# Optimization experiments

Measured on AMD Instinct MI355X. Metric: run time of the kernel, lower is better.

The kernel has to match this reference:

```python
import jax, jax.numpy as jnp
from jax import lax
import numpy as np

VOCAB, EMB = 50000, 300
HID, NCLS = 100, 20
BATCH, SEQ = 128, 512
P_DROP = 0.5


def setup_inputs() -> dict:
    key = jax.random.key(0)
    ks = jax.random.split(key, 8)
    s_e = 1.0 / np.sqrt(EMB)
    s_h = 1.0 / np.sqrt(HID)
    return {
        "inputs_batch": jax.random.randint(ks[0], (BATCH, SEQ), 0, VOCAB, dtype=jnp.int64)
        if jax.config.jax_enable_x64 else jax.random.randint(ks[0], (BATCH, SEQ), 0, VOCAB, dtype=jnp.int32),
        "emb_table": jax.random.normal(ks[1], (VOCAB, EMB), dtype=jnp.float32),
        # GRUCell params (torch layout): gates order [r, z, n]
        "w_ih": jax.random.uniform(ks[2], (3 * HID, EMB), jnp.float32, -s_h, s_h),
        "w_hh": jax.random.uniform(ks[3], (3 * HID, HID), jnp.float32, -s_h, s_h),
        "b_ih": jax.random.uniform(ks[4], (3 * HID,), jnp.float32, -s_h, s_h),
        "b_hh": jax.random.uniform(ks[5], (3 * HID,), jnp.float32, -s_h, s_h),
        "w_lin": jax.random.uniform(ks[6], (NCLS, HID), jnp.float32, -s_h, s_h),
        "b_lin": jax.random.uniform(ks[7], (NCLS,), jnp.float32, -s_h, s_h),
    }


def reference(inputs_batch, emb_table, w_ih, w_hh, b_ih, b_hh, w_lin, b_lin):
    B, S = inputs_batch.shape
    H = w_hh.shape[1]
    keep = 1.0 - P_DROP
    dk1, dk2 = jax.random.split(jax.random.key(42))

    z_embed = emb_table[inputs_batch]                       # [B, S, E]
    m1 = jax.random.bernoulli(dk1, keep, z_embed.shape)     # dropout1 mask
    z_embed = jnp.where(m1, z_embed / keep, 0.0)
    x_seq = jnp.swapaxes(z_embed, 0, 1)                     # [S, B, E]
    m2 = jax.random.bernoulli(dk2, keep, (S, B, H))         # per-step dropout2 masks

    def step(h, inp):
        x, m = inp
        gi = x @ w_ih.T + b_ih                              # [B, 3H]
        gh = h @ w_hh.T + b_hh
        i_r, i_z, i_n = jnp.split(gi, 3, axis=-1)
        h_r, h_z, h_n = jnp.split(gh, 3, axis=-1)
        r = jax.nn.sigmoid(i_r + h_r)
        zg = jax.nn.sigmoid(i_z + h_z)
        n = jnp.tanh(i_n + r * h_n)
        h_new = (1.0 - zg) * n + zg * h
        h_d = jnp.where(m, h_new / keep, 0.0)
        y = jax.nn.log_softmax(h_d @ w_lin.T + b_lin, axis=1)  # [B, C]
        return h_new, y

    h0 = jnp.zeros((B, H), dtype=x_seq.dtype)
    _, ys = lax.scan(step, h0, (x_seq, m2))                 # ys: [S, B, C]
    return jnp.transpose(ys, (1, 2, 0))                     # [B, C, S]
```

## Files before the change

kernel.cpp:

```cpp
#include <hip/hip_runtime.h>
#include <hip/hip_bf16.h>
#include <cstdint>

#define BATCH 128
#define SEQ   512
#define EMB   300
#define HID   100
#define G3    300
#define NCLS  20
#define NROWS (SEQ * BATCH)

#define M1_WORDS 614400
#define M2_WORDS 204800

typedef __attribute__((ext_vector_type(4))) float f32x4;
typedef __attribute__((ext_vector_type(8))) short s16x8;
typedef __fp16 h16x2 __attribute__((ext_vector_type(2)));

__host__ __device__ __forceinline__ void threefry2x32(uint32_t k0, uint32_t k1,
                                                      uint32_t x0, uint32_t x1,
                                                      uint32_t* o0, uint32_t* o1) {
  uint32_t ks2 = k0 ^ k1 ^ 0x1BD11BDAu;
  x0 += k0; x1 += k1;
#define TFR(r) { x0 += x1; x1 = (x1 << (r)) | (x1 >> (32 - (r))); x1 ^= x0; }
  TFR(13) TFR(15) TFR(26) TFR(6)  x0 += k1;  x1 += ks2 + 1u;
  TFR(17) TFR(29) TFR(16) TFR(24) x0 += ks2; x1 += k0 + 2u;
  TFR(13) TFR(15) TFR(26) TFR(6)  x0 += k0;  x1 += k1 + 3u;
  TFR(17) TFR(29) TFR(16) TFR(24) x0 += k1;  x1 += ks2 + 4u;
  TFR(13) TFR(15) TFR(26) TFR(6)  x0 += ks2; x1 += k0 + 5u;
#undef TFR
  *o0 = x0; *o1 = x1;
}

__device__ __forceinline__ uint32_t rand_bits32(uint32_t ka, uint32_t kb, uint32_t flat) {
  uint32_t a, b;
  threefry2x32(ka, kb, 0u, flat, &a, &b);
  return a ^ b;
}

__device__ __forceinline__ short f2bf(float f) {
  union { float f; uint32_t u; } c; c.f = f;
  uint32_t u = c.u;
  return (short)((u + 0x7FFFu + ((u >> 16) & 1u)) >> 16);
}

__device__ __forceinline__ void bar_lds() {
  __asm__ __volatile__("s_waitcnt lgkmcnt(0)" ::: "memory");
  __builtin_amdgcn_s_barrier();
  __asm__ __volatile__("" ::: "memory");
}

__global__ __launch_bounds__(256) void k_mask(uint32_t* __restrict__ M1w,
                                              uint32_t* __restrict__ M2w,
                                              uint32_t k1a, uint32_t k1b,
                                              uint32_t k2a, uint32_t k2b) {
  const int i = blockIdx.x * 256 + threadIdx.x;
  uint32_t ka, kb, base;
  uint32_t* dst;
  if (i < M1_WORDS) { ka = k1a; kb = k1b; base = (uint32_t)i * 32u; dst = M1w + i; }
  else { ka = k2a; kb = k2b; base = (uint32_t)(i - M1_WORDS) * 32u; dst = M2w + (i - M1_WORDS); }
  uint32_t w = 0u;
#pragma unroll
  for (int j = 0; j < 32; ++j) {
    uint32_t bits = rand_bits32(ka, kb, base + (uint32_t)j);
    w |= ((~bits) >> 31) << j;
  }
  *dst = w;
}

__global__ __launch_bounds__(256) void k_prepw(const float* __restrict__ w_ih,
                                               short* __restrict__ Wb) {
  int i8 = (blockIdx.x * 256 + threadIdx.x) * 8;
  if (i8 >= 304 * 320) return;
  short o[8];
#pragma unroll
  for (int j = 0; j < 8; ++j) {
    int pos = i8 + j;
    int n = pos / 320, k = pos - (pos / 320) * 320;
    float v = (n < 300 && k < 300) ? w_ih[(size_t)n * EMB + k] : 0.f;
    o[j] = f2bf(v);
  }
  *(s16x8*)(Wb + i8) = *(s16x8*)o;
}

__global__ __launch_bounds__(512) void k_gi7(const int* __restrict__ inputs,
                                             const float* __restrict__ emb,
                                             const short* __restrict__ Wb,
                                             const float* __restrict__ b_ih,
                                             const uint32_t* __restrict__ M1w,
                                             float* __restrict__ GI) {
  __shared__ short As[128 * 40];
  __shared__ short Bs[304 * 40];
  __shared__ int idxs[128];
  const int t = threadIdx.x;
  const int s = blockIdx.x;
  const int lane = t & 63, wave = t >> 6;
  const int wr = wave & 1;
  const int wc = wave >> 1;
  const int ml = lane & 15, quad = lane >> 4;
  const int arow = t >> 2;
  const int akq = t & 3;

  if (t < 128) idxs[t] = inputs[t * SEQ + s];
  __syncthreads();

  const int nfr = (wc < 3) ? 5 : 4;
  f32x4 acc[4][5];
#pragma unroll
  for (int i = 0; i < 4; ++i)
#pragma unroll
    for (int j = 0; j < 5; ++j) acc[i][j] = (f32x4){0.f, 0.f, 0.f, 0.f};

  const int myidx = idxs[arow];

  for (int c = 0; c < 10; ++c) {
    const int e0 = c * 32 + akq * 8;
    float xa[8];
#pragma unroll
    for (int j = 0; j < 8; ++j) xa[j] = 0.f;
    if (e0 + 7 < 300) {
#pragma unroll
      for (int q4 = 0; q4 < 2; ++q4) {
        float4 v = *(const float4*)(emb + (size_t)myidx * EMB + e0 + q4 * 4);
        xa[q4 * 4 + 0] = v.x; xa[q4 * 4 + 1] = v.y; xa[q4 * 4 + 2] = v.z; xa[q4 * 4 + 3] = v.w;
      }
    } else if (e0 < 300) {
#pragma unroll
      for (int j = 0; j < 8; ++j) {
        int e = e0 + j;
        if (e < 300) xa[j] = emb[(size_t)myidx * EMB + e];
      }
    }
    uint32_t mb = 0;
    if (e0 < 300) {
      uint32_t base = (uint32_t)((arow * SEQ + s) * EMB + e0);
      uint64_t mw = (uint64_t)M1w[base >> 5] | ((uint64_t)M1w[(base >> 5) + 1] << 32);
      mb = (uint32_t)(mw >> (base & 31));
    }
    short sa[8];
#pragma unroll
    for (int j = 0; j < 8; ++j)
      sa[j] = f2bf(((mb >> j) & 1u) ? xa[j] * 2.f : 0.f);
    s16x8 bv0, bv1, bv2;
    {
      int i0 = t;
      bv0 = *(const s16x8*)(Wb + (size_t)(i0 >> 2) * 320 + c * 32 + (i0 & 3) * 8);
      int i1 = t + 512;
      bv1 = *(const s16x8*)(Wb + (size_t)(i1 >> 2) * 320 + c * 32 + (i1 & 3) * 8);
      if (t < 192) {
        int i2 = t + 1024;
        bv2 = *(const s16x8*)(Wb + (size_t)(i2 >> 2) * 320 + c * 32 + (i2 & 3) * 8);
      }
    }
    if (c > 0) __syncthreads();
    *(s16x8*)&As[arow * 40 + akq * 8] = *(s16x8*)&sa[0];
    {
      int i0 = t;       *(s16x8*)&Bs[(i0 >> 2) * 40 + (i0 & 3) * 8] = bv0;
      int i1 = t + 512; *(s16x8*)&Bs[(i1 >> 2) * 40 + (i1 & 3) * 8] = bv1;
      if (t < 192) { int i2 = t + 1024; *(s16x8*)&Bs[(i2 >> 2) * 40 + (i2 & 3) * 8] = bv2; }
    }
    __syncthreads();
    s16x8 af[4];
#pragma unroll
    for (int mt = 0; mt < 4; ++mt)
      af[mt] = *(const s16x8*)&As[(wr * 64 + mt * 16 + ml) * 40 + quad * 8];
#pragma unroll
    for (int j = 0; j < 5; ++j) {
      if (j < nfr) {
        int nt = wc + 4 * j;
        s16x8 bf = *(const s16x8*)&Bs[(nt * 16 + ml) * 40 + quad * 8];
#pragma unroll
        for (int mt = 0; mt < 4; ++mt)
          acc[mt][j] = __builtin_amdgcn_mfma_f32_16x16x32_bf16(af[mt], bf, acc[mt][j], 0, 0, 0);
      }
    }
  }

#pragma unroll
  for (int j = 0; j < 5; ++j) {
    if (j < nfr) {
      int n = (wc + 4 * j) * 16 + ml;
      if (n < 300) {
        float bias = b_ih[n];
#pragma unroll
        for (int mt = 0; mt < 4; ++mt) {
#pragma unroll
          for (int i = 0; i < 4; ++i) {
            int brow = wr * 64 + mt * 16 + quad * 4 + i;
            GI[(size_t)(s * BATCH + brow) * G3 + n] = acc[mt][j][i] + bias;
          }
        }
      }
    }
  }
}

__global__ __launch_bounds__(512, 1) void k_rnn12(const float* __restrict__ GI,
                                                  const float* __restrict__ w_hh,
                                                  const float* __restrict__ b_hh,
                                                  const uint8_t* __restrict__ M2,
                                                  float* __restrict__ Hd) {
  __shared__ __align__(16) uint32_t hp_s[2][64];
  const int t = threadIdx.x, b = blockIdx.x;
  const int u = t >> 2, ks = t & 3;
  const bool act = (u < 100);
  const bool gate = act && (ks == 0);
  const int uc = act ? u : 99;
  const int kplo = (ks < 2) ? ks * 13 : 26 + (ks - 2) * 12;
  const int np = (ks < 2) ? 13 : 12;

  const float* rowR = w_hh + (size_t)uc * HID;
  const float* rowZ = w_hh + (size_t)(uc + 100) * HID;
  const float* rowN = w_hh + (size_t)(uc + 200) * HID;
  const h16x2 z2 = (h16x2){(__fp16)0.f, (__fp16)0.f};
  h16x2 wR[13], wZ[13], wN[13];
#pragma unroll
  for (int j = 0; j < 13; ++j) {
    if (j < np) {
      int o = 2 * (kplo + j);
      wR[j] = __builtin_amdgcn_cvt_pkrtz(rowR[o], rowR[o + 1]);
      wZ[j] = __builtin_amdgcn_cvt_pkrtz(rowZ[o], rowZ[o + 1]);
      wN[j] = __builtin_amdgcn_cvt_pkrtz(rowN[o], rowN[o + 1]);
    } else { wR[j] = z2; wZ[j] = z2; wN[j] = z2; }
  }

  float bR0 = 0.f, bZ0 = 0.f, bN0 = 0.f;
  float gcR = 0.f, gcZ = 0.f, gcN = 0.f;
  float g1R = 0.f, g1Z = 0.f, g1N = 0.f;
  uint8_t mc = 0, m1 = 0;
  if (gate) {
    bR0 = b_hh[u]; bZ0 = b_hh[100 + u]; bN0 = b_hh[200 + u];
    const float* g0 = GI + (size_t)b * G3;
    gcR = g0[u]; gcZ = g0[100 + u]; gcN = g0[200 + u];
    mc = M2[(uint32_t)(b * HID + u) >> 3];
    const float* gp1 = GI + (size_t)(BATCH + b) * G3;
    g1R = gp1[u]; g1Z = gp1[100 + u]; g1N = gp1[200 + u];
    m1 = M2[(uint32_t)((BATCH + b) * HID + u) >> 3];
  }
  const int p = u >> 1;
  const int sidx = (p < 13) ? 0 : (p < 26) ? 1 : (p < 38) ? 2 : 3;
  const int spos = p - ((sidx < 2) ? sidx * 13 : 26 + (sidx - 2) * 12);
  const int hidx = (sidx * 16 + spos) * 2 + (u & 1);

  if (t < 128) ((uint32_t*)hp_s)[t] = 0u;
  float hprev = 0.f;
  __syncthreads();

#define QPX(x, c) __builtin_bit_cast(float, __builtin_amdgcn_mov_dpp( \
    __builtin_bit_cast(int, (x)), (c), 0xF, 0xF, true))
#define DOT_S(J, W) { h16x2 hh = __builtin_bit_cast(h16x2, (W)); \
    sR = __builtin_amdgcn_fdot2(wR[J], hh, sR, false); \
    sZ = __builtin_amdgcn_fdot2(wZ[J], hh, sZ, false); \
    sN = __builtin_amdgcn_fdot2(wN[J], hh, sN, false); }
#define DOT_T(J, W) { h16x2 hh = __builtin_bit_cast(h16x2, (W)); \
    tR = __builtin_amdgcn_fdot2(wR[J], hh, tR, false); \
    tZ = __builtin_amdgcn_fdot2(wZ[J], hh, tZ, false); \
    tN = __builtin_amdgcn_fdot2(wN[J], hh, tN, false); }

#pragma unroll 2
  for (int s = 0; s < SEQ; ++s) {
    float g2R = 0.f, g2Z = 0.f, g2N = 0.f;
    uint8_t m2b = 0;
    if (gate) {
      int sn = (s + 2 < SEQ) ? s + 2 : SEQ - 1;
      const float* gp = GI + (size_t)(sn * BATCH + b) * G3;
      g2R = gp[u]; g2Z = gp[100 + u]; g2N = gp[200 + u];
      m2b = M2[(uint32_t)((sn * BATCH + b) * HID + u) >> 3];
    }
    if (act) {
      float sR = bR0, sZ = bZ0, sN = bN0;
      float tR = 0.f, tZ = 0.f, tN = 0.f;
      const uint32_t* hb = &hp_s[s & 1][0] + (ks << 4);
      uint4 h0 = *(const uint4*)hb;
      uint4 h1 = *(const uint4*)(hb + 4);
      uint4 h2 = *(const uint4*)(hb + 8);
      uint32_t h3 = hb[12];
      DOT_S(0, h0.x)  DOT_S(1, h0.y)  DOT_S(2, h0.z)  DOT_S(3, h0.w)
      DOT_S(4, h1.x)  DOT_S(5, h1.y)
      DOT_T(6, h1.z)  DOT_T(7, h1.w)
      DOT_T(8, h2.x)  DOT_T(9, h2.y)  DOT_T(10, h2.z) DOT_T(11, h2.w)
      DOT_T(12, h3)
      sR += tR; sZ += tZ; sN += tN;
      sR += QPX(sR, 0xB1); sZ += QPX(sZ, 0xB1); sN += QPX(sN, 0xB1);
      sR += QPX(sR, 0x4E); sZ += QPX(sZ, 0x4E); sN += QPX(sN, 0x4E);
      if (gate) {
        float r = 1.f / (1.f + __expf(-(gcR + sR)));
        float z = 1.f / (1.f + __expf(-(gcZ + sZ)));
        float xn = gcN + r * sN;
        float e2 = __expf(2.f * fabsf(xn));
        float n = copysignf(1.f - 2.f / (e2 + 1.f), xn);
        float hnew = (1.f - z) * n + z * hprev;
        hprev = hnew;
        uint32_t fl = (uint32_t)((s * BATCH + b) * HID + u);
        float hd = ((mc >> (fl & 7)) & 1u) ? hnew * 2.f : 0.f;
        Hd[(size_t)(b * SEQ + s) * HID + u] = hd;
        ((__fp16*)&hp_s[(s & 1) ^ 1][0])[hidx] = (__fp16)hnew;
      }
    }
    gcR = g1R; gcZ = g1Z; gcN = g1N; mc = m1;
    g1R = g2R; g1Z = g2Z; g1N = g2N; m1 = m2b;
    bar_lds();
  }
#undef DOT_S
#undef DOT_T
#undef QPX
}

__global__ __launch_bounds__(64) void k_out(const float* __restrict__ Hd,
                                            const float* __restrict__ w_lin,
                                            const float* __restrict__ b_lin,
                                            float* __restrict__ out) {
  __shared__ float Wl[NCLS * HID];
  __shared__ float bl[NCLS];
  const int t = threadIdx.x;
  for (int i = t; i < NCLS * HID; i += 64) Wl[i] = w_lin[i];
  if (t < NCLS) bl[t] = b_lin[t];
  __syncthreads();

  const int r0 = (blockIdx.x * 64 + t) * 4;
  float acc[4][NCLS];
#pragma unroll
  for (int r = 0; r < 4; ++r)
#pragma unroll
    for (int c = 0; c < NCLS; ++c) acc[r][c] = bl[c];

  for (int k = 0; k < HID; k += 4) {
    float4 h0 = *(const float4*)(Hd + (size_t)(r0 + 0) * HID + k);
    float4 h1 = *(const float4*)(Hd + (size_t)(r0 + 1) * HID + k);
    float4 h2 = *(const float4*)(Hd + (size_t)(r0 + 2) * HID + k);
    float4 h3 = *(const float4*)(Hd + (size_t)(r0 + 3) * HID + k);
#pragma unroll
    for (int c = 0; c < NCLS; ++c) {
      float4 w4 = *(const float4*)&Wl[c * HID + k];
      acc[0][c] += h0.x * w4.x + h0.y * w4.y + h0.z * w4.z + h0.w * w4.w;
      acc[1][c] += h1.x * w4.x + h1.y * w4.y + h1.z * w4.z + h1.w * w4.w;
      acc[2][c] += h2.x * w4.x + h2.y * w4.y + h2.z * w4.z + h2.w * w4.w;
      acc[3][c] += h3.x * w4.x + h3.y * w4.y + h3.z * w4.z + h3.w * w4.w;
    }
  }

  float lse[4];
#pragma unroll
  for (int r = 0; r < 4; ++r) {
    float mx = acc[r][0];
#pragma unroll
    for (int c = 1; c < NCLS; ++c) mx = fmaxf(mx, acc[r][c]);
    float se = 0.f;
#pragma unroll
    for (int c = 0; c < NCLS; ++c) se += __expf(acc[r][c] - mx);
    lse[r] = mx + __logf(se);
  }
  const int b = r0 >> 9, s0 = r0 & 511;
#pragma unroll
  for (int c = 0; c < NCLS; ++c) {
    float4 o = make_float4(acc[0][c] - lse[0], acc[1][c] - lse[1],
                           acc[2][c] - lse[2], acc[3][c] - lse[3]);
    *(float4*)(out + (size_t)(b * NCLS + c) * SEQ + s0) = o;
  }
}

extern "C" void kernel_launch(void* const* d_in, const int* in_sizes, int n_in,
                              void* d_out, int out_size, void* d_ws, size_t ws_size,
                              hipStream_t stream) {
  const int*   inputs = (const int*)d_in[0];
  const float* emb    = (const float*)d_in[1];
  const float* w_ih   = (const float*)d_in[2];
  const float* w_hh   = (const float*)d_in[3];
  const float* b_ih   = (const float*)d_in[4];
  const float* b_hh   = (const float*)d_in[5];
  const float* w_lin  = (const float*)d_in[6];
  const float* b_lin  = (const float*)d_in[7];
  float* out = (float*)d_out;

  float* GI = (float*)d_ws;
  float* Hd = GI + (size_t)NROWS * G3;
  uint8_t* M1 = (uint8_t*)(Hd + (size_t)NROWS * HID);
  uint8_t* M2 = M1 + (size_t)M1_WORDS * 4;
  short* Wb = (short*)(M2 + (size_t)M2_WORDS * 4);

  uint32_t dk1a, dk1b, dk2a, dk2b;
  threefry2x32(0u, 42u, 0u, 0u, &dk1a, &dk1b);
  threefry2x32(0u, 42u, 0u, 1u, &dk2a, &dk2b);

  k_mask<<<(M1_WORDS + M2_WORDS) / 256, 256, 0, stream>>>(
      (uint32_t*)M1, (uint32_t*)M2, dk1a, dk1b, dk2a, dk2b);
  k_prepw<<<(304 * 320 / 8 + 255) / 256, 256, 0, stream>>>(w_ih, Wb);
  k_gi7<<<512, 512, 0, stream>>>(inputs, emb, Wb, b_ih, (const uint32_t*)M1, GI);
  k_rnn12<<<BATCH, 512, 0, stream>>>(GI, w_hh, b_hh, M2, Hd);
  k_out<<<256, 64, 0, stream>>>(Hd, w_lin, b_lin, out);
}
```

Measured before the change: 562.4 us.

## Compute GRU recurrent matvec with MFMA instead of fdot2 plus DPP reduction

The recurrent h·W_hh product per step moves from per-thread fdot2 chains with a cross-lane DPP reduction onto MFMA 16x16x32 f16 instructions. Each of 7 waves covers 16 hidden units, and the A operand holds h broadcast in row 0, so only one output row is useful. The block shrinks from 512 to 448 threads and the hidden state is stored as a plain f16 vector in LDS. This removes the DPP shuffle reduction from the serial step, but adds MFMA latency (12 chained MFMAs) to the critical path and wastes most of each MFMA's rows.

```diff
diff --git a/kernel.cpp b/kernel.cpp
--- a/kernel.cpp
+++ b/kernel.cpp
@@ -15,7 +15,7 @@
 
 typedef __attribute__((ext_vector_type(4))) float f32x4;
 typedef __attribute__((ext_vector_type(8))) short s16x8;
-typedef __fp16 h16x2 __attribute__((ext_vector_type(2)));
+typedef __fp16 f16x8 __attribute__((ext_vector_type(8)));
 
 __host__ __device__ __forceinline__ void threefry2x32(uint32_t k0, uint32_t k1,
                                                       uint32_t x0, uint32_t x1,
@@ -195,41 +195,41 @@
   }
 }
 
-__global__ __launch_bounds__(512, 1) void k_rnn12(const float* __restrict__ GI,
+__global__ __launch_bounds__(448, 1) void k_rnn13(const float* __restrict__ GI,
                                                   const float* __restrict__ w_hh,
                                                   const float* __restrict__ b_hh,
                                                   const uint8_t* __restrict__ M2,
                                                   float* __restrict__ Hd) {
-  __shared__ __align__(16) uint32_t hp_s[2][64];
+  __shared__ __align__(16) __fp16 hb[2][128];
   const int t = threadIdx.x, b = blockIdx.x;
-  const int u = t >> 2, ks = t & 3;
-  const bool act = (u < 100);
-  const bool gate = act && (ks == 0);
-  const int uc = act ? u : 99;
-  const int kplo = (ks < 2) ? ks * 13 : 26 + (ks - 2) * 12;
-  const int np = (ks < 2) ? 13 : 12;
-
-  const float* rowR = w_hh + (size_t)uc * HID;
-  const float* rowZ = w_hh + (size_t)(uc + 100) * HID;
-  const float* rowN = w_hh + (size_t)(uc + 200) * HID;
-  const h16x2 z2 = (h16x2){(__fp16)0.f, (__fp16)0.f};
-  h16x2 wR[13], wZ[13], wN[13];
-#pragma unroll
-  for (int j = 0; j < 13; ++j) {
-    if (j < np) {
-      int o = 2 * (kplo + j);
-      wR[j] = __builtin_amdgcn_cvt_pkrtz(rowR[o], rowR[o + 1]);
-      wZ[j] = __builtin_amdgcn_cvt_pkrtz(rowZ[o], rowZ[o + 1]);
-      wN[j] = __builtin_amdgcn_cvt_pkrtz(rowN[o], rowN[o + 1]);
-    } else { wR[j] = z2; wZ[j] = z2; wN[j] = z2; }
-  }
-
-  float bR0 = 0.f, bZ0 = 0.f, bN0 = 0.f;
+  const int lane = t & 63, w = t >> 6;
+  const int ml = lane & 15, kg = lane >> 4;
+  const int u = w * 16 + ml;
+  const bool gate = (lane < 16) && (u < 100);
+  const int urow = (u < 100) ? u : 99;
+
+  f16x8 Bf[3][4];
+#pragma unroll
+  for (int g = 0; g < 3; ++g) {
+    const float* wr = w_hh + (size_t)(g * 100 + urow) * HID;
+#pragma unroll
+    for (int kt = 0; kt < 4; ++kt) {
+      f16x8 v;
+#pragma unroll
+      for (int j = 0; j < 8; ++j) {
+        int k = kt * 32 + kg * 8 + j;
+        v[j] = (__fp16)((k < 100) ? wr[k] : 0.f);
+      }
+      Bf[g][kt] = v;
+    }
+  }
+
+  const float biasR = b_hh[urow], biasZ = b_hh[100 + urow], biasN = b_hh[200 + urow];
+
   float gcR = 0.f, gcZ = 0.f, gcN = 0.f;
   float g1R = 0.f, g1Z = 0.f, g1N = 0.f;
   uint8_t mc = 0, m1 = 0;
   if (gate) {
-    bR0 = b_hh[u]; bZ0 = b_hh[100 + u]; bN0 = b_hh[200 + u];
     const float* g0 = GI + (size_t)b * G3;
     gcR = g0[u]; gcZ = g0[100 + u]; gcN = g0[200 + u];
     mc = M2[(uint32_t)(b * HID + u) >> 3];
@@ -237,27 +237,16 @@
     g1R = gp1[u]; g1Z = gp1[100 + u]; g1N = gp1[200 + u];
     m1 = M2[(uint32_t)((BATCH + b) * HID + u) >> 3];
   }
-  const int p = u >> 1;
-  const int sidx = (p < 13) ? 0 : (p < 26) ? 1 : (p < 38) ? 2 : 3;
-  const int spos = p - ((sidx < 2) ? sidx * 13 : 26 + (sidx - 2) * 12);
-  const int hidx = (sidx * 16 + spos) * 2 + (u & 1);
-
-  if (t < 128) ((uint32_t*)hp_s)[t] = 0u;
+
+  if (t < 128) ((uint32_t*)hb)[t] = 0u;
   float hprev = 0.f;
   __syncthreads();
 
-#define QPX(x, c) __builtin_bit_cast(float, __builtin_amdgcn_mov_dpp( \
-    __builtin_bit_cast(int, (x)), (c), 0xF, 0xF, true))
-#define DOT_S(J, W) { h16x2 hh = __builtin_bit_cast(h16x2, (W)); \
-    sR = __builtin_amdgcn_fdot2(wR[J], hh, sR, false); \
-    sZ = __builtin_amdgcn_fdot2(wZ[J], hh, sZ, false); \
-    sN = __builtin_amdgcn_fdot2(wN[J], hh, sN, false); }
-#define DOT_T(J, W) { h16x2 hh = __builtin_bit_cast(h16x2, (W)); \
-    tR = __builtin_amdgcn_fdot2(wR[J], hh, tR, false); \
-    tZ = __builtin_amdgcn_fdot2(wZ[J], hh, tZ, false); \
-    tN = __builtin_amdgcn_fdot2(wN[J], hh, tN, false); }
-
-#pragma unroll 2
+#define MM3(AF, KT) \
+  aR = __builtin_amdgcn_mfma_f32_16x16x32_f16((AF), Bf[0][KT], aR, 0, 0, 0); \
+  aZ = __builtin_amdgcn_mfma_f32_16x16x32_f16((AF), Bf[1][KT], aZ, 0, 0, 0); \
+  aN = __builtin_amdgcn_mfma_f32_16x16x32_f16((AF), Bf[2][KT], aN, 0, 0, 0);
+
   for (int s = 0; s < SEQ; ++s) {
     float g2R = 0.f, g2Z = 0.f, g2N = 0.f;
     uint8_t m2b = 0;
@@ -267,43 +256,36 @@
       g2R = gp[u]; g2Z = gp[100 + u]; g2N = gp[200 + u];
       m2b = M2[(uint32_t)((sn * BATCH + b) * HID + u) >> 3];
     }
-    if (act) {
-      float sR = bR0, sZ = bZ0, sN = bN0;
-      float tR = 0.f, tZ = 0.f, tN = 0.f;
-      const uint32_t* hb = &hp_s[s & 1][0] + (ks << 4);
-      uint4 h0 = *(const uint4*)hb;
-      uint4 h1 = *(const uint4*)(hb + 4);
-      uint4 h2 = *(const uint4*)(hb + 8);
-      uint32_t h3 = hb[12];
-      DOT_S(0, h0.x)  DOT_S(1, h0.y)  DOT_S(2, h0.z)  DOT_S(3, h0.w)
-      DOT_S(4, h1.x)  DOT_S(5, h1.y)
-      DOT_T(6, h1.z)  DOT_T(7, h1.w)
-      DOT_T(8, h2.x)  DOT_T(9, h2.y)  DOT_T(10, h2.z) DOT_T(11, h2.w)
-      DOT_T(12, h3)
-      sR += tR; sZ += tZ; sN += tN;
-      sR += QPX(sR, 0xB1); sZ += QPX(sZ, 0xB1); sN += QPX(sN, 0xB1);
-      sR += QPX(sR, 0x4E); sZ += QPX(sZ, 0x4E); sN += QPX(sN, 0x4E);
-      if (gate) {
-        float r = 1.f / (1.f + __expf(-(gcR + sR)));
-        float z = 1.f / (1.f + __expf(-(gcZ + sZ)));
-        float xn = gcN + r * sN;
-        float e2 = __expf(2.f * fabsf(xn));
-        float n = copysignf(1.f - 2.f / (e2 + 1.f), xn);
-        float hnew = (1.f - z) * n + z * hprev;
-        hprev = hnew;
-        uint32_t fl = (uint32_t)((s * BATCH + b) * HID + u);
-        float hd = ((mc >> (fl & 7)) & 1u) ? hnew * 2.f : 0.f;
-        Hd[(size_t)(b * SEQ + s) * HID + u] = hd;
-        ((__fp16*)&hp_s[(s & 1) ^ 1][0])[hidx] = (__fp16)hnew;
-      }
+
+    const __fp16* hp = &hb[s & 1][0];
+    const f16x8 A0 = *(const f16x8*)(hp + 0 * 32 + kg * 8);
+    const f16x8 A1 = *(const f16x8*)(hp + 1 * 32 + kg * 8);
+    const f16x8 A2 = *(const f16x8*)(hp + 2 * 32 + kg * 8);
+    const f16x8 A3 = *(const f16x8*)(hp + 3 * 32 + kg * 8);
+
+    f32x4 aR = (f32x4){biasR, 0.f, 0.f, 0.f};
+    f32x4 aZ = (f32x4){biasZ, 0.f, 0.f, 0.f};
+    f32x4 aN = (f32x4){biasN, 0.f, 0.f, 0.f};
+    MM3(A0, 0) MM3(A1, 1) MM3(A2, 2) MM3(A3, 3)
+
+    if (gate) {
+      float r = 1.f / (1.f + __expf(-(gcR + aR[0])));
+      float z = 1.f / (1.f + __expf(-(gcZ + aZ[0])));
+      float xn = gcN + r * aN[0];
+      float e2 = __expf(2.f * fabsf(xn));
+      float n = copysignf(1.f - 2.f / (e2 + 1.f), xn);
+      float hnew = (1.f - z) * n + z * hprev;
+      hprev = hnew;
+      uint32_t fl = (uint32_t)((s * BATCH + b) * HID + u);
+      float hd = ((mc >> (fl & 7)) & 1u) ? hnew * 2.f : 0.f;
+      Hd[(size_t)(b * SEQ + s) * HID + u] = hd;
+      hb[(s & 1) ^ 1][u] = (__fp16)hnew;
     }
     gcR = g1R; gcZ = g1Z; gcN = g1N; mc = m1;
     g1R = g2R; g1Z = g2Z; g1N = g2N; m1 = m2b;
     bar_lds();
   }
-#undef DOT_S
-#undef DOT_T
-#undef QPX
+#undef MM3
 }
 
 __global__ __launch_bounds__(64) void k_out(const float* __restrict__ Hd,
@@ -386,6 +368,6 @@
       (uint32_t*)M1, (uint32_t*)M2, dk1a, dk1b, dk2a, dk2b);
   k_prepw<<<(304 * 320 / 8 + 255) / 256, 256, 0, stream>>>(w_ih, Wb);
   k_gi7<<<512, 512, 0, stream>>>(inputs, emb, Wb, b_ih, (const uint32_t*)M1, GI);
-  k_rnn12<<<BATCH, 512, 0, stream>>>(GI, w_hh, b_hh, M2, Hd);
+  k_rnn13<<<BATCH, 448, 0, stream>>>(GI, w_hh, b_hh, M2, Hd);
   k_out<<<256, 64, 0, stream>>>(Hd, w_lin, b_lin, out);
 }
```

Result: slower. 633.3 us (+12.6%).

## Buffer hidden-state history in LDS and apply dropout/store after recurrence

Applied to the files above, without the earlier changes.

The RNN kernel now keeps all 512 fp16 hidden-state vectors in a 128KB LDS history buffer instead of a double buffer. The per-step mask load, dropout select and global Hd store move out of the serial recurrence into a parallel epilogue that reads the history and the mask bits. The prefetch distance drops from two steps to one, and the step-0 matvec is skipped. Hd values now come from fp16-rounded h rather than fp32. The large LDS footprint limits occupancy, though only one block runs per CU anyway.

```diff
diff --git a/kernel.cpp b/kernel.cpp
--- a/kernel.cpp
+++ b/kernel.cpp
@@ -195,12 +195,12 @@
   }
 }
 
-__global__ __launch_bounds__(512, 1) void k_rnn12(const float* __restrict__ GI,
+__global__ __launch_bounds__(512, 1) void k_rnn14(const float* __restrict__ GI,
                                                   const float* __restrict__ w_hh,
                                                   const float* __restrict__ b_hh,
                                                   const uint8_t* __restrict__ M2,
                                                   float* __restrict__ Hd) {
-  __shared__ __align__(16) uint32_t hp_s[2][64];
+  __shared__ __align__(16) uint32_t hist[512][64];
   const int t = threadIdx.x, b = blockIdx.x;
   const int u = t >> 2, ks = t & 3;
   const bool act = (u < 100);
@@ -226,25 +226,20 @@
 
   float bR0 = 0.f, bZ0 = 0.f, bN0 = 0.f;
   float gcR = 0.f, gcZ = 0.f, gcN = 0.f;
-  float g1R = 0.f, g1Z = 0.f, g1N = 0.f;
-  uint8_t mc = 0, m1 = 0;
   if (gate) {
     bR0 = b_hh[u]; bZ0 = b_hh[100 + u]; bN0 = b_hh[200 + u];
     const float* g0 = GI + (size_t)b * G3;
     gcR = g0[u]; gcZ = g0[100 + u]; gcN = g0[200 + u];
-    mc = M2[(uint32_t)(b * HID + u) >> 3];
-    const float* gp1 = GI + (size_t)(BATCH + b) * G3;
-    g1R = gp1[u]; g1Z = gp1[100 + u]; g1N = gp1[200 + u];
-    m1 = M2[(uint32_t)((BATCH + b) * HID + u) >> 3];
   }
   const int p = u >> 1;
   const int sidx = (p < 13) ? 0 : (p < 26) ? 1 : (p < 38) ? 2 : 3;
   const int spos = p - ((sidx < 2) ? sidx * 13 : 26 + (sidx - 2) * 12);
   const int hidx = (sidx * 16 + spos) * 2 + (u & 1);
 
-  if (t < 128) ((uint32_t*)hp_s)[t] = 0u;
+  hist[t][44] = 0u;
+  hist[t][60] = 0u;
   float hprev = 0.f;
-  __syncthreads();
+  bar_lds();
 
 #define QPX(x, c) __builtin_bit_cast(float, __builtin_amdgcn_mov_dpp( \
     __builtin_bit_cast(int, (x)), (c), 0xF, 0xF, true))
@@ -257,30 +252,29 @@
     tZ = __builtin_amdgcn_fdot2(wZ[J], hh, tZ, false); \
     tN = __builtin_amdgcn_fdot2(wN[J], hh, tN, false); }
 
-#pragma unroll 2
   for (int s = 0; s < SEQ; ++s) {
-    float g2R = 0.f, g2Z = 0.f, g2N = 0.f;
-    uint8_t m2b = 0;
+    float gnR = 0.f, gnZ = 0.f, gnN = 0.f;
     if (gate) {
-      int sn = (s + 2 < SEQ) ? s + 2 : SEQ - 1;
+      int sn = (s + 1 < SEQ) ? s + 1 : s;
       const float* gp = GI + (size_t)(sn * BATCH + b) * G3;
-      g2R = gp[u]; g2Z = gp[100 + u]; g2N = gp[200 + u];
-      m2b = M2[(uint32_t)((sn * BATCH + b) * HID + u) >> 3];
+      gnR = gp[u]; gnZ = gp[100 + u]; gnN = gp[200 + u];
     }
     if (act) {
       float sR = bR0, sZ = bZ0, sN = bN0;
-      float tR = 0.f, tZ = 0.f, tN = 0.f;
-      const uint32_t* hb = &hp_s[s & 1][0] + (ks << 4);
-      uint4 h0 = *(const uint4*)hb;
-      uint4 h1 = *(const uint4*)(hb + 4);
-      uint4 h2 = *(const uint4*)(hb + 8);
-      uint32_t h3 = hb[12];
-      DOT_S(0, h0.x)  DOT_S(1, h0.y)  DOT_S(2, h0.z)  DOT_S(3, h0.w)
-      DOT_S(4, h1.x)  DOT_S(5, h1.y)
-      DOT_T(6, h1.z)  DOT_T(7, h1.w)
-      DOT_T(8, h2.x)  DOT_T(9, h2.y)  DOT_T(10, h2.z) DOT_T(11, h2.w)
-      DOT_T(12, h3)
-      sR += tR; sZ += tZ; sN += tN;
+      if (s > 0) {
+        float tR = 0.f, tZ = 0.f, tN = 0.f;
+        const uint32_t* hb = &hist[s - 1][0] + (ks << 4);
+        uint4 h0 = *(const uint4*)hb;
+        uint4 h1 = *(const uint4*)(hb + 4);
+        uint4 h2 = *(const uint4*)(hb + 8);
+        uint32_t h3 = hb[12];
+        DOT_S(0, h0.x)  DOT_S(1, h0.y)  DOT_S(2, h0.z)  DOT_S(3, h0.w)
+        DOT_S(4, h1.x)  DOT_S(5, h1.y)
+        DOT_T(6, h1.z)  DOT_T(7, h1.w)
+        DOT_T(8, h2.x)  DOT_T(9, h2.y)  DOT_T(10, h2.z) DOT_T(11, h2.w)
+        DOT_T(12, h3)
+        sR += tR; sZ += tZ; sN += tN;
+      }
       sR += QPX(sR, 0xB1); sZ += QPX(sZ, 0xB1); sN += QPX(sN, 0xB1);
       sR += QPX(sR, 0x4E); sZ += QPX(sZ, 0x4E); sN += QPX(sN, 0x4E);
       if (gate) {
@@ -291,19 +285,39 @@
         float n = copysignf(1.f - 2.f / (e2 + 1.f), xn);
         float hnew = (1.f - z) * n + z * hprev;
         hprev = hnew;
-        uint32_t fl = (uint32_t)((s * BATCH + b) * HID + u);
-        float hd = ((mc >> (fl & 7)) & 1u) ? hnew * 2.f : 0.f;
-        Hd[(size_t)(b * SEQ + s) * HID + u] = hd;
-        ((__fp16*)&hp_s[(s & 1) ^ 1][0])[hidx] = (__fp16)hnew;
-      }
-    }
-    gcR = g1R; gcZ = g1Z; gcN = g1N; mc = m1;
-    g1R = g2R; g1Z = g2Z; g1N = g2N; m1 = m2b;
+        ((__fp16*)&hist[s][0])[hidx] = (__fp16)hnew;
+      }
+    }
+    gcR = gnR; gcZ = gnZ; gcN = gnN;
     bar_lds();
   }
 #undef DOT_S
 #undef DOT_T
 #undef QPX
+
+  {
+    const int fq = t & 3;
+    const int fs_base = t >> 2;
+    const int fkplo = (fq < 2) ? fq * 13 : 26 + (fq - 2) * 12;
+    const int fnp = (fq < 2) ? 13 : 12;
+    const int fu0 = 2 * fkplo;
+    const uint32_t* Mw = (const uint32_t*)M2;
+    for (int pass = 0; pass < 4; ++pass) {
+      const int s = fs_base + pass * 128;
+      const uint32_t* hr = &hist[s][fq * 16];
+      uint32_t bit0 = (uint32_t)((s * BATCH + b) * HID + fu0);
+      uint64_t mw = (uint64_t)Mw[bit0 >> 5] | ((uint64_t)Mw[(bit0 >> 5) + 1] << 32);
+      uint32_t mb = (uint32_t)(mw >> (bit0 & 31));
+      float* dst = Hd + (size_t)(b * SEQ + s) * HID + fu0;
+      for (int d = 0; d < fnp; ++d) {
+        uint32_t pw = hr[d];
+        h16x2 hp = __builtin_bit_cast(h16x2, pw);
+        float h0 = (float)hp[0], h1 = (float)hp[1];
+        dst[2 * d]     = ((mb >> (2 * d)) & 1u)     ? h0 * 2.f : 0.f;
+        dst[2 * d + 1] = ((mb >> (2 * d + 1)) & 1u) ? h1 * 2.f : 0.f;
+      }
+    }
+  }
 }
 
 __global__ __launch_bounds__(64) void k_out(const float* __restrict__ Hd,
@@ -386,6 +400,6 @@
       (uint32_t*)M1, (uint32_t*)M2, dk1a, dk1b, dk2a, dk2b);
   k_prepw<<<(304 * 320 / 8 + 255) / 256, 256, 0, stream>>>(w_ih, Wb);
   k_gi7<<<512, 512, 0, stream>>>(inputs, emb, Wb, b_ih, (const uint32_t*)M1, GI);
-  k_rnn12<<<BATCH, 512, 0, stream>>>(GI, w_hh, b_hh, M2, Hd);
+  k_rnn14<<<BATCH, 512, 0, stream>>>(GI, w_hh, b_hh, M2, Hd);
   k_out<<<256, 64, 0, stream>>>(Hd, w_lin, b_lin, out);
 }
```

Measured after the change: 578.2 us. 1.03x slower.
